# Kernel optimization log

Hardware: AMD Instinct MI355X
Metric: run time of the kernel (lower is better)

The kernel has to match this reference:

```python
import jax, jax.numpy as jnp
import numpy as np

B, L = 2, 8192
HID, HEADS, STATE, K = 1024, 16, 16, 3
HD = HID // HEADS  # head dim = 64


def setup_inputs() -> dict:
    key = jax.random.key(0)
    ks = jax.random.split(key, 4)
    u = jax.random.normal(ks[0], (B, L, 3 * HID), dtype=jnp.float32)
    short_filter_weight = jax.random.normal(ks[1], (3 * HID, 1, K), dtype=jnp.float32)
    log_poles = -jnp.abs(jax.random.normal(ks[2], (1, STATE, 1), dtype=jnp.float32))
    residues = jax.random.normal(ks[3], (1, STATE), dtype=jnp.float32)
    D = jnp.zeros((HID,), dtype=jnp.float32)
    return {"u": u, "short_filter_weight": short_filter_weight,
            "log_poles": log_poles, "residues": residues, "D": D}


def _causal_dconv(x, w):
    # x: (B, C, L), w: (C, 1, K). Cross-correlation (matches torch conv1d)
    # with left pad K-1 == torch padding=K-1 then truncating [..., :L].
    return jax.lax.conv_general_dilated(
        x, w, window_strides=(1,), padding=[(K - 1, 0)],
        dimension_numbers=("NCH", "OIH", "NCH"),
        feature_group_count=x.shape[1])


def _bidir_dconv(x, w):
    # bidirectional FIR: causal conv + anti-causal conv (same filter on the
    # time-reversed signal, reversed back), summed
    fwd = _causal_dconv(x, w)
    rev = _causal_dconv(x[..., ::-1], w)[..., ::-1]
    return fwd + rev


def _fftconv(x, H, fft_size):
    # causal long conv via 2L-point FFT (zero-padded -> linear convolution)
    X = jnp.fft.rfft(x, n=fft_size)
    return jnp.fft.irfft(X * H, n=fft_size)[..., : x.shape[-1]]


def reference(u, short_filter_weight, log_poles, residues, D):
    Bx, Lx, _ = u.shape
    u_t = jnp.transpose(u, (0, 2, 1))                 # (B, 3*HID, L)
    z_pre = _bidir_dconv(u_t, short_filter_weight)    # (B, 3*HID, L)

    # column_split: (B, HEADS, 3*HD, L) -> x2, x1, v each (B, HID, L)
    z = z_pre.reshape(Bx, HEADS, 3 * HD, Lx)
    x2 = z[:, :, :HD].reshape(Bx, HID, Lx)
    x1 = z[:, :, HD:2 * HD].reshape(Bx, HID, Lx)
    v = z[:, :, 2 * HD:].reshape(Bx, HID, Lx)
    x1v = x1 * v

    # implicit long filter from pole/residue parameterization: h (1, 1, L)
    t = jnp.arange(Lx, dtype=jnp.float32)[None, None]           # (1,1,L)
    h = (residues[..., None] * jnp.exp(log_poles * t)).sum(axis=1)[None]

    fft_size = 2 * Lx
    H = jnp.fft.rfft(h.astype(jnp.float32), n=fft_size)          # (1,1,L+1)
    # bidirectional long conv: causal + anti-causal branches
    y = (_fftconv(x1v, H, fft_size)
         + _fftconv(x1v[..., ::-1], H, fft_size)[..., ::-1])

    # skip term and output gate
    y = (y + x1v * D[:, None]) * x2                   # (B, HID, L)
    return jnp.transpose(y, (0, 2, 1))                # (B, L, HID)
```

## Files before the change

kernel.cpp:

```cpp
#include <hip/hip_runtime.h>
#include <cstdint>
#include <cstddef>


#define Bn 2
#define Ln 8192
#define HIDn 1024
#define HEADSn 16
#define STATEn 16
#define THIDn 3072

typedef __attribute__((ext_vector_type(2))) float f32x2;

__device__ __forceinline__ float ldu(const float* __restrict__ base, int t) {
    return ((unsigned)t < (unsigned)Ln) ? base[(size_t)t * THIDn] : 0.0f;
}

template <int CH>
__global__ __launch_bounds__(64, 4) void hyena_phaseA(
    const float* __restrict__ u, const float* __restrict__ sfw,
    const float* __restrict__ lp,
    float* __restrict__ carryF, float* __restrict__ carryG) {
    const int j = threadIdx.x;
    const int chunk = blockIdx.x;
    const int h = blockIdx.y;
    const int b = blockIdx.z;
    const int c1 = h * 192 + 64 + j;
    const int cv = c1 + 64;
    const int t0 = chunk * CH;
    const int t1 = t0 + CH - 1;

    const float* u1 = u + (size_t)b * Ln * THIDn + c1;
    const float* uv = u + (size_t)b * Ln * THIDn + cv;
    const float w10 = sfw[c1 * 3 + 0], w11 = sfw[c1 * 3 + 1], w12 = 2.0f * sfw[c1 * 3 + 2];
    const float wv0 = sfw[cv * 3 + 0], wv1 = sfw[cv * 3 + 1], wv2 = 2.0f * sfw[cv * 3 + 2];

    f32x2 p2[8];
#pragma unroll
    for (int i = 0; i < 8; ++i) p2[i] = (f32x2){expf(lp[2 * i]), expf(lp[2 * i + 1])};

    const int i = h * 64 + j;
    const int gch = b * HIDn + i;
    const size_t base = ((size_t)chunk * (Bn * HIDn) + gch) * 16;

    {
        f32x2 f2[8];
#pragma unroll
        for (int s = 0; s < 8; ++s) f2[s] = (f32x2){0.0f, 0.0f};
        float a0 = ldu(u1, t0 - 2), a1 = ldu(u1, t0 - 1), a2 = ldu(u1, t0), a3 = ldu(u1, t0 + 1);
        float v0 = ldu(uv, t0 - 2), v1 = ldu(uv, t0 - 1), v2 = ldu(uv, t0), v3 = ldu(uv, t0 + 1);
#pragma unroll 8
        for (int tt = 0; tt < CH; ++tt) {
            const int t = t0 + tt;
            const float a4 = ldu(u1, t + 2);
            const float v4 = ldu(uv, t + 2);
            const float z1 = fmaf(w10, a0 + a4, fmaf(w11, a1 + a3, w12 * a2));
            const float zv = fmaf(wv0, v0 + v4, fmaf(wv1, v1 + v3, wv2 * v2));
            const float x = z1 * zv;
            const f32x2 x2 = (f32x2){x, x};
#pragma unroll
            for (int s = 0; s < 8; ++s) f2[s] = __builtin_elementwise_fma(p2[s], f2[s], x2);
            a0 = a1; a1 = a2; a2 = a3; a3 = a4;
            v0 = v1; v1 = v2; v2 = v3; v3 = v4;
        }
        f32x2* cF2 = (f32x2*)(carryF + base);
#pragma unroll
        for (int s = 0; s < 8; ++s) cF2[s] = f2[s];
    }

    {
        f32x2 g2[8];
#pragma unroll
        for (int s = 0; s < 8; ++s) g2[s] = (f32x2){0.0f, 0.0f};
        float a4 = ldu(u1, t1 + 2), a3 = ldu(u1, t1 + 1), a2 = ldu(u1, t1), a1 = ldu(u1, t1 - 1);
        float v4 = ldu(uv, t1 + 2), v3 = ldu(uv, t1 + 1), v2 = ldu(uv, t1), v1 = ldu(uv, t1 - 1);
#pragma unroll 8
        for (int tt = CH - 1; tt >= 0; --tt) {
            const int t = t0 + tt;
            const float a0 = ldu(u1, t - 2);
            const float v0 = ldu(uv, t - 2);
            const float z1 = fmaf(w10, a0 + a4, fmaf(w11, a1 + a3, w12 * a2));
            const float zv = fmaf(wv0, v0 + v4, fmaf(wv1, v1 + v3, wv2 * v2));
            const float x = z1 * zv;
            const f32x2 x2 = (f32x2){x, x};
#pragma unroll
            for (int s = 0; s < 8; ++s) g2[s] = __builtin_elementwise_fma(p2[s], g2[s], x2);
            a4 = a3; a3 = a2; a2 = a1; a1 = a0;
            v4 = v3; v3 = v2; v2 = v1; v1 = v0;
        }
        f32x2* cG2 = (f32x2*)(carryG + base);
#pragma unroll
        for (int s = 0; s < 8; ++s) cG2[s] = g2[s];
    }
}

template <int CH>
__global__ __launch_bounds__(256) void hyena_phaseB(
    const float* __restrict__ lp,
    float* __restrict__ carryF, float* __restrict__ carryG) {
    constexpr int NC = Ln / CH;
    constexpr int UB = 16;
    const int dir = blockIdx.x >> 7;
    const int ht = ((blockIdx.x & 127) << 8) + threadIdx.x;
    const int s = ht & 15;
    const int gch = ht >> 4;
    const float pCH = expf(lp[s] * (float)CH);
    float c = 0.0f;
    if (dir == 0) {
        for (int k0 = 0; k0 < NC; k0 += UB) {
            float loc[UB];
#pragma unroll
            for (int q = 0; q < UB; ++q)
                loc[q] = carryF[((size_t)(k0 + q) * (Bn * HIDn) + gch) * 16 + s];
#pragma unroll
            for (int q = 0; q < UB; ++q) {
                carryF[((size_t)(k0 + q) * (Bn * HIDn) + gch) * 16 + s] = c;
                c = fmaf(pCH, c, loc[q]);
            }
        }
    } else {
        for (int k0 = NC - UB; k0 >= 0; k0 -= UB) {
            float loc[UB];
#pragma unroll
            for (int q = UB - 1; q >= 0; --q)
                loc[q] = carryG[((size_t)(k0 + q) * (Bn * HIDn) + gch) * 16 + s];
#pragma unroll
            for (int q = UB - 1; q >= 0; --q) {
                carryG[((size_t)(k0 + q) * (Bn * HIDn) + gch) * 16 + s] = c;
                c = fmaf(pCH, c, loc[q]);
            }
        }
    }
}

template <int CH>
__global__ __launch_bounds__(64, 4) void hyena_phaseC(
    const float* __restrict__ u, const float* __restrict__ sfw,
    const float* __restrict__ lp, const float* __restrict__ res,
    const float* __restrict__ Dp,
    const float* __restrict__ carryF, const float* __restrict__ carryG,
    float* __restrict__ out) {
    const int j = threadIdx.x;
    const int chunk = blockIdx.x;
    const int h = blockIdx.y;
    const int b = blockIdx.z;
    const int c2 = h * 192 + j;
    const int c1 = c2 + 64;
    const int cv = c2 + 128;
    const int i = h * 64 + j;
    const int gch = b * HIDn + i;
    const int t0 = chunk * CH;
    const int t1 = t0 + CH - 1;

    const float* u2 = u + (size_t)b * Ln * THIDn + c2;
    const float* u1 = u + (size_t)b * Ln * THIDn + c1;
    const float* uv = u + (size_t)b * Ln * THIDn + cv;
    float* op = out + (size_t)b * Ln * HIDn + i;
    const float w20 = sfw[c2 * 3 + 0], w21 = sfw[c2 * 3 + 1], w22 = 2.0f * sfw[c2 * 3 + 2];
    const float w10 = sfw[c1 * 3 + 0], w11 = sfw[c1 * 3 + 1], w12 = 2.0f * sfw[c1 * 3 + 2];
    const float wv0 = sfw[cv * 3 + 0], wv1 = sfw[cv * 3 + 1], wv2 = 2.0f * sfw[cv * 3 + 2];

    f32x2 p2[8];
#pragma unroll
    for (int s = 0; s < 8; ++s) p2[s] = (f32x2){expf(lp[2 * s]), expf(lp[2 * s + 1])};
    float rr[STATEn];
#pragma unroll
    for (int s = 0; s < STATEn; ++s) rr[s] = res[s];

    const size_t cbase = ((size_t)chunk * (Bn * HIDn) + gch) * 16;

    {
        f32x2 f2[8];
        const f32x2* cF2 = (const f32x2*)(carryF + cbase);
#pragma unroll
        for (int s = 0; s < 8; ++s) f2[s] = cF2[s];
        float a0 = ldu(u1, t0 - 2), a1 = ldu(u1, t0 - 1), a2 = ldu(u1, t0), a3 = ldu(u1, t0 + 1);
        float v0 = ldu(uv, t0 - 2), v1 = ldu(uv, t0 - 1), v2 = ldu(uv, t0), v3 = ldu(uv, t0 + 1);
#pragma unroll 8
        for (int tt = 0; tt < CH; ++tt) {
            const int t = t0 + tt;
            const float a4 = ldu(u1, t + 2);
            const float v4 = ldu(uv, t + 2);
            const float z1 = fmaf(w10, a0 + a4, fmaf(w11, a1 + a3, w12 * a2));
            const float zv = fmaf(wv0, v0 + v4, fmaf(wv1, v1 + v3, wv2 * v2));
            const float x = z1 * zv;
            const f32x2 xb = (f32x2){x, x};
#pragma unroll
            for (int s = 0; s < 8; ++s) f2[s] = __builtin_elementwise_fma(p2[s], f2[s], xb);
            float acc0 = rr[0] * f2[0].x, acc1 = rr[1] * f2[0].y;
            float acc2 = rr[2] * f2[1].x, acc3 = rr[3] * f2[1].y;
#pragma unroll
            for (int s = 2; s < 8; s += 2) {
                acc0 = fmaf(rr[2 * s + 0], f2[s].x, acc0);
                acc1 = fmaf(rr[2 * s + 1], f2[s].y, acc1);
                acc2 = fmaf(rr[2 * s + 2], f2[s + 1].x, acc2);
                acc3 = fmaf(rr[2 * s + 3], f2[s + 1].y, acc3);
            }
            op[(size_t)t * HIDn] = (acc0 + acc1) + (acc2 + acc3);
            a0 = a1; a1 = a2; a2 = a3; a3 = a4;
            v0 = v1; v1 = v2; v2 = v3; v3 = v4;
        }
    }

    {
        f32x2 g2[8];
        const f32x2* cG2 = (const f32x2*)(carryG + cbase);
#pragma unroll
        for (int s = 0; s < 8; ++s) g2[s] = cG2[s];
        const float dI = Dp[i];
        float a4 = ldu(u1, t1 + 2), a3 = ldu(u1, t1 + 1), a2 = ldu(u1, t1), a1 = ldu(u1, t1 - 1);
        float v4 = ldu(uv, t1 + 2), v3 = ldu(uv, t1 + 1), v2 = ldu(uv, t1), v1 = ldu(uv, t1 - 1);
        float e4 = ldu(u2, t1 + 2), e3 = ldu(u2, t1 + 1), e2 = ldu(u2, t1), e1 = ldu(u2, t1 - 1);
#pragma unroll 8
        for (int tt = CH - 1; tt >= 0; --tt) {
            const int t = t0 + tt;
            const float yc = op[(size_t)t * HIDn];
            const float a0 = ldu(u1, t - 2);
            const float v0 = ldu(uv, t - 2);
            const float e0 = ldu(u2, t - 2);
            const float z1 = fmaf(w10, a0 + a4, fmaf(w11, a1 + a3, w12 * a2));
            const float zv = fmaf(wv0, v0 + v4, fmaf(wv1, v1 + v3, wv2 * v2));
            const float z2 = fmaf(w20, e0 + e4, fmaf(w21, e1 + e3, w22 * e2));
            const float x = z1 * zv;
            const f32x2 xb = (f32x2){x, x};
#pragma unroll
            for (int s = 0; s < 8; ++s) g2[s] = __builtin_elementwise_fma(p2[s], g2[s], xb);
            float acc0 = rr[0] * g2[0].x, acc1 = rr[1] * g2[0].y;
            float acc2 = rr[2] * g2[1].x, acc3 = rr[3] * g2[1].y;
#pragma unroll
            for (int s = 2; s < 8; s += 2) {
                acc0 = fmaf(rr[2 * s + 0], g2[s].x, acc0);
                acc1 = fmaf(rr[2 * s + 1], g2[s].y, acc1);
                acc2 = fmaf(rr[2 * s + 2], g2[s + 1].x, acc2);
                acc3 = fmaf(rr[2 * s + 3], g2[s + 1].y, acc3);
            }
            const float ya = (acc0 + acc1) + (acc2 + acc3);
            op[(size_t)t * HIDn] = (yc + ya + dI * x) * z2;
            a4 = a3; a3 = a2; a2 = a1; a1 = a0;
            v4 = v3; v3 = v2; v2 = v1; v1 = v0;
            e4 = e3; e3 = e2; e2 = e1; e1 = e0;
        }
    }
}

template <int CH>
static void run_all(const float* u, const float* sfw, const float* lp,
                    const float* res, const float* Dp, float* out,
                    void* ws, hipStream_t stream) {
    constexpr int NC = Ln / CH;
    float* carryF = (float*)ws;
    float* carryG = carryF + (size_t)NC * (Bn * HIDn) * 16;
    dim3 grid(NC, HEADSn, Bn);
    hipLaunchKernelGGL((hyena_phaseA<CH>), grid, dim3(64), 0, stream,
                       u, sfw, lp, carryF, carryG);
    hipLaunchKernelGGL((hyena_phaseB<CH>), dim3(256), dim3(256), 0, stream,
                       lp, carryF, carryG);
    hipLaunchKernelGGL((hyena_phaseC<CH>), grid, dim3(64), 0, stream,
                       u, sfw, lp, res, Dp, carryF, carryG, out);
}

extern "C" void kernel_launch(void* const* d_in, const int* in_sizes, int n_in,
                              void* d_out, int out_size, void* d_ws, size_t ws_size,
                              hipStream_t stream) {
    const float* u   = (const float*)d_in[0];
    const float* sfw = (const float*)d_in[1];
    const float* lp  = (const float*)d_in[2];
    const float* res = (const float*)d_in[3];
    const float* Dp  = (const float*)d_in[4];
    float* out = (float*)d_out;

    const size_t need64 = ((size_t)1 << 31) / 64;
    if (ws_size >= need64)            run_all<64>(u, sfw, lp, res, Dp, out, d_ws, stream);
    else if (ws_size >= need64 / 2)   run_all<128>(u, sfw, lp, res, Dp, out, d_ws, stream);
    else if (ws_size >= need64 / 4)   run_all<256>(u, sfw, lp, res, Dp, out, d_ws, stream);
    else                              run_all<512>(u, sfw, lp, res, Dp, out, d_ws, stream);
}
```

Before: 416.3 us.

## Pack four chunks per block, drop interior bounds checks, vectorize conv, allow smaller chunks

```diff
diff --git a/kernel.cpp b/kernel.cpp
--- a/kernel.cpp
+++ b/kernel.cpp
@@ -11,87 +11,103 @@
 #define THIDn 3072
 
 typedef __attribute__((ext_vector_type(2))) float f32x2;
-
-__device__ __forceinline__ float ldu(const float* __restrict__ base, int t) {
-    return ((unsigned)t < (unsigned)Ln) ? base[(size_t)t * THIDn] : 0.0f;
+typedef __attribute__((ext_vector_type(4))) float f32x4;
+
+template <bool G>
+__device__ __forceinline__ float ldc(const float* __restrict__ base, int t) {
+    if constexpr (G) return ((unsigned)t < (unsigned)Ln) ? base[(size_t)t * THIDn] : 0.0f;
+    else return base[(size_t)t * THIDn];
+}
+
+template <int CH, bool G>
+__device__ __forceinline__ void phaseA_body(
+    const float* __restrict__ u1, const float* __restrict__ uv,
+    const f32x2 W0, const f32x2 W1, const f32x2 W2,
+    const f32x2 (&p2)[8], int t0,
+    float* __restrict__ cF, float* __restrict__ cG) {
+    const int t1 = t0 + CH - 1;
+    {
+        f32x2 f2[8];
+#pragma unroll
+        for (int s = 0; s < 8; ++s) f2[s] = (f32x2){0.0f, 0.0f};
+        f32x2 av0 = {ldc<G>(u1, t0 - 2), ldc<G>(uv, t0 - 2)};
+        f32x2 av1 = {ldc<G>(u1, t0 - 1), ldc<G>(uv, t0 - 1)};
+        f32x2 av2 = {ldc<G>(u1, t0    ), ldc<G>(uv, t0    )};
+        f32x2 av3 = {ldc<G>(u1, t0 + 1), ldc<G>(uv, t0 + 1)};
+#pragma unroll 8
+        for (int tt = 0; tt < CH; ++tt) {
+            const int t = t0 + tt;
+            const f32x2 av4 = {ldc<G>(u1, t + 2), ldc<G>(uv, t + 2)};
+            const f32x2 z = __builtin_elementwise_fma(W0, av0 + av4,
+                              __builtin_elementwise_fma(W1, av1 + av3, W2 * av2));
+            const float x = z.x * z.y;
+            const f32x2 xb = {x, x};
+#pragma unroll
+            for (int s = 0; s < 8; ++s) f2[s] = __builtin_elementwise_fma(p2[s], f2[s], xb);
+            av0 = av1; av1 = av2; av2 = av3; av3 = av4;
+        }
+        f32x4* o = (f32x4*)cF;
+#pragma unroll
+        for (int s = 0; s < 4; ++s)
+            o[s] = (f32x4){f2[2 * s].x, f2[2 * s].y, f2[2 * s + 1].x, f2[2 * s + 1].y};
+    }
+    {
+        f32x2 g2[8];
+#pragma unroll
+        for (int s = 0; s < 8; ++s) g2[s] = (f32x2){0.0f, 0.0f};
+        f32x2 av4 = {ldc<G>(u1, t1 + 2), ldc<G>(uv, t1 + 2)};
+        f32x2 av3 = {ldc<G>(u1, t1 + 1), ldc<G>(uv, t1 + 1)};
+        f32x2 av2 = {ldc<G>(u1, t1    ), ldc<G>(uv, t1    )};
+        f32x2 av1 = {ldc<G>(u1, t1 - 1), ldc<G>(uv, t1 - 1)};
+#pragma unroll 8
+        for (int tt = CH - 1; tt >= 0; --tt) {
+            const int t = t0 + tt;
+            const f32x2 av0 = {ldc<G>(u1, t - 2), ldc<G>(uv, t - 2)};
+            const f32x2 z = __builtin_elementwise_fma(W0, av0 + av4,
+                              __builtin_elementwise_fma(W1, av1 + av3, W2 * av2));
+            const float x = z.x * z.y;
+            const f32x2 xb = {x, x};
+#pragma unroll
+            for (int s = 0; s < 8; ++s) g2[s] = __builtin_elementwise_fma(p2[s], g2[s], xb);
+            av4 = av3; av3 = av2; av2 = av1; av1 = av0;
+        }
+        f32x4* o = (f32x4*)cG;
+#pragma unroll
+        for (int s = 0; s < 4; ++s)
+            o[s] = (f32x4){g2[2 * s].x, g2[2 * s].y, g2[2 * s + 1].x, g2[2 * s + 1].y};
+    }
 }
 
 template <int CH>
-__global__ __launch_bounds__(64, 4) void hyena_phaseA(
+__global__ __launch_bounds__(256, 8) void hyena_phaseA(
     const float* __restrict__ u, const float* __restrict__ sfw,
     const float* __restrict__ lp,
     float* __restrict__ carryF, float* __restrict__ carryG) {
-    const int j = threadIdx.x;
-    const int chunk = blockIdx.x;
+    constexpr int NC = Ln / CH;
+    const int lane = threadIdx.x & 63;
+    const int chunk = (blockIdx.x << 2) + (threadIdx.x >> 6);
     const int h = blockIdx.y;
     const int b = blockIdx.z;
-    const int c1 = h * 192 + 64 + j;
+    const int c1 = h * 192 + 64 + lane;
     const int cv = c1 + 64;
     const int t0 = chunk * CH;
-    const int t1 = t0 + CH - 1;
 
     const float* u1 = u + (size_t)b * Ln * THIDn + c1;
     const float* uv = u + (size_t)b * Ln * THIDn + cv;
-    const float w10 = sfw[c1 * 3 + 0], w11 = sfw[c1 * 3 + 1], w12 = 2.0f * sfw[c1 * 3 + 2];
-    const float wv0 = sfw[cv * 3 + 0], wv1 = sfw[cv * 3 + 1], wv2 = 2.0f * sfw[cv * 3 + 2];
-
+    const f32x2 W0 = {sfw[c1 * 3 + 0], sfw[cv * 3 + 0]};
+    const f32x2 W1 = {sfw[c1 * 3 + 1], sfw[cv * 3 + 1]};
+    const f32x2 W2 = {2.0f * sfw[c1 * 3 + 2], 2.0f * sfw[cv * 3 + 2]};
     f32x2 p2[8];
 #pragma unroll
-    for (int i = 0; i < 8; ++i) p2[i] = (f32x2){expf(lp[2 * i]), expf(lp[2 * i + 1])};
-
-    const int i = h * 64 + j;
-    const int gch = b * HIDn + i;
-    const size_t base = ((size_t)chunk * (Bn * HIDn) + gch) * 16;
-
-    {
-        f32x2 f2[8];
-#pragma unroll
-        for (int s = 0; s < 8; ++s) f2[s] = (f32x2){0.0f, 0.0f};
-        float a0 = ldu(u1, t0 - 2), a1 = ldu(u1, t0 - 1), a2 = ldu(u1, t0), a3 = ldu(u1, t0 + 1);
-        float v0 = ldu(uv, t0 - 2), v1 = ldu(uv, t0 - 1), v2 = ldu(uv, t0), v3 = ldu(uv, t0 + 1);
-#pragma unroll 8
-        for (int tt = 0; tt < CH; ++tt) {
-            const int t = t0 + tt;
-            const float a4 = ldu(u1, t + 2);
-            const float v4 = ldu(uv, t + 2);
-            const float z1 = fmaf(w10, a0 + a4, fmaf(w11, a1 + a3, w12 * a2));
-            const float zv = fmaf(wv0, v0 + v4, fmaf(wv1, v1 + v3, wv2 * v2));
-            const float x = z1 * zv;
-            const f32x2 x2 = (f32x2){x, x};
-#pragma unroll
-            for (int s = 0; s < 8; ++s) f2[s] = __builtin_elementwise_fma(p2[s], f2[s], x2);
-            a0 = a1; a1 = a2; a2 = a3; a3 = a4;
-            v0 = v1; v1 = v2; v2 = v3; v3 = v4;
-        }
-        f32x2* cF2 = (f32x2*)(carryF + base);
-#pragma unroll
-        for (int s = 0; s < 8; ++s) cF2[s] = f2[s];
-    }
-
-    {
-        f32x2 g2[8];
-#pragma unroll
-        for (int s = 0; s < 8; ++s) g2[s] = (f32x2){0.0f, 0.0f};
-        float a4 = ldu(u1, t1 + 2), a3 = ldu(u1, t1 + 1), a2 = ldu(u1, t1), a1 = ldu(u1, t1 - 1);
-        float v4 = ldu(uv, t1 + 2), v3 = ldu(uv, t1 + 1), v2 = ldu(uv, t1), v1 = ldu(uv, t1 - 1);
-#pragma unroll 8
-        for (int tt = CH - 1; tt >= 0; --tt) {
-            const int t = t0 + tt;
-            const float a0 = ldu(u1, t - 2);
-            const float v0 = ldu(uv, t - 2);
-            const float z1 = fmaf(w10, a0 + a4, fmaf(w11, a1 + a3, w12 * a2));
-            const float zv = fmaf(wv0, v0 + v4, fmaf(wv1, v1 + v3, wv2 * v2));
-            const float x = z1 * zv;
-            const f32x2 x2 = (f32x2){x, x};
-#pragma unroll
-            for (int s = 0; s < 8; ++s) g2[s] = __builtin_elementwise_fma(p2[s], g2[s], x2);
-            a4 = a3; a3 = a2; a2 = a1; a1 = a0;
-            v4 = v3; v3 = v2; v2 = v1; v1 = v0;
-        }
-        f32x2* cG2 = (f32x2*)(carryG + base);
-#pragma unroll
-        for (int s = 0; s < 8; ++s) cG2[s] = g2[s];
-    }
+    for (int s = 0; s < 8; ++s) p2[s] = (f32x2){expf(lp[2 * s]), expf(lp[2 * s + 1])};
+
+    const int gch = b * HIDn + h * 64 + lane;
+    const size_t cbase = ((size_t)chunk * (Bn * HIDn) + gch) * 16;
+
+    if (chunk >= 1 && chunk <= NC - 2)
+        phaseA_body<CH, false>(u1, uv, W0, W1, W2, p2, t0, carryF + cbase, carryG + cbase);
+    else
+        phaseA_body<CH, true>(u1, uv, W0, W1, W2, p2, t0, carryF + cbase, carryG + cbase);
 }
 
 template <int CH>
@@ -99,7 +115,7 @@
     const float* __restrict__ lp,
     float* __restrict__ carryF, float* __restrict__ carryG) {
     constexpr int NC = Ln / CH;
-    constexpr int UB = 16;
+    constexpr int UB = (NC >= 32) ? 32 : 16;
     const int dir = blockIdx.x >> 7;
     const int ht = ((blockIdx.x & 127) << 8) + threadIdx.x;
     const int s = ht & 15;
@@ -133,114 +149,137 @@
     }
 }
 
+template <int CH, bool G>
+__device__ __forceinline__ void phaseC_body(
+    const float* __restrict__ u2, const float* __restrict__ u1, const float* __restrict__ uv,
+    float* __restrict__ op,
+    const f32x2 W0, const f32x2 W1, const f32x2 W2,
+    const float w20, const float w21, const float w22,
+    const f32x2 (&p2)[8], const f32x2 (&rr2)[8], const float dI,
+    const float* __restrict__ cF, const float* __restrict__ cG, int t0) {
+    const int t1 = t0 + CH - 1;
+    {
+        f32x2 f2[8];
+        const f32x4* ci = (const f32x4*)cF;
+#pragma unroll
+        for (int s = 0; s < 4; ++s) {
+            const f32x4 q = ci[s];
+            f2[2 * s]     = (f32x2){q.x, q.y};
+            f2[2 * s + 1] = (f32x2){q.z, q.w};
+        }
+        f32x2 av0 = {ldc<G>(u1, t0 - 2), ldc<G>(uv, t0 - 2)};
+        f32x2 av1 = {ldc<G>(u1, t0 - 1), ldc<G>(uv, t0 - 1)};
+        f32x2 av2 = {ldc<G>(u1, t0    ), ldc<G>(uv, t0    )};
+        f32x2 av3 = {ldc<G>(u1, t0 + 1), ldc<G>(uv, t0 + 1)};
+#pragma unroll 8
+        for (int tt = 0; tt < CH; ++tt) {
+            const int t = t0 + tt;
+            const f32x2 av4 = {ldc<G>(u1, t + 2), ldc<G>(uv, t + 2)};
+            const f32x2 z = __builtin_elementwise_fma(W0, av0 + av4,
+                              __builtin_elementwise_fma(W1, av1 + av3, W2 * av2));
+            const float x = z.x * z.y;
+            const f32x2 xb = {x, x};
+#pragma unroll
+            for (int s = 0; s < 8; ++s) f2[s] = __builtin_elementwise_fma(p2[s], f2[s], xb);
+            f32x2 accA = rr2[0] * f2[0];
+            f32x2 accB = rr2[1] * f2[1];
+#pragma unroll
+            for (int s = 2; s < 8; s += 2) {
+                accA = __builtin_elementwise_fma(rr2[s], f2[s], accA);
+                accB = __builtin_elementwise_fma(rr2[s + 1], f2[s + 1], accB);
+            }
+            const f32x2 acc = accA + accB;
+            op[(size_t)t * HIDn] = acc.x + acc.y;
+            av0 = av1; av1 = av2; av2 = av3; av3 = av4;
+        }
+    }
+    {
+        f32x2 g2[8];
+        const f32x4* ci = (const f32x4*)cG;
+#pragma unroll
+        for (int s = 0; s < 4; ++s) {
+            const f32x4 q = ci[s];
+            g2[2 * s]     = (f32x2){q.x, q.y};
+            g2[2 * s + 1] = (f32x2){q.z, q.w};
+        }
+        f32x2 av4 = {ldc<G>(u1, t1 + 2), ldc<G>(uv, t1 + 2)};
+        f32x2 av3 = {ldc<G>(u1, t1 + 1), ldc<G>(uv, t1 + 1)};
+        f32x2 av2 = {ldc<G>(u1, t1    ), ldc<G>(uv, t1    )};
+        f32x2 av1 = {ldc<G>(u1, t1 - 1), ldc<G>(uv, t1 - 1)};
+        float e4 = ldc<G>(u2, t1 + 2), e3 = ldc<G>(u2, t1 + 1);
+        float e2 = ldc<G>(u2, t1), e1 = ldc<G>(u2, t1 - 1);
+#pragma unroll 8
+        for (int tt = CH - 1; tt >= 0; --tt) {
+            const int t = t0 + tt;
+            const float yc = op[(size_t)t * HIDn];
+            const f32x2 av0 = {ldc<G>(u1, t - 2), ldc<G>(uv, t - 2)};
+            const float e0 = ldc<G>(u2, t - 2);
+            const f32x2 z = __builtin_elementwise_fma(W0, av0 + av4,
+                              __builtin_elementwise_fma(W1, av1 + av3, W2 * av2));
+            const float z2 = fmaf(w20, e0 + e4, fmaf(w21, e1 + e3, w22 * e2));
+            const float x = z.x * z.y;
+            const f32x2 xb = {x, x};
+#pragma unroll
+            for (int s = 0; s < 8; ++s) g2[s] = __builtin_elementwise_fma(p2[s], g2[s], xb);
+            f32x2 accA = rr2[0] * g2[0];
+            f32x2 accB = rr2[1] * g2[1];
+#pragma unroll
+            for (int s = 2; s < 8; s += 2) {
+                accA = __builtin_elementwise_fma(rr2[s], g2[s], accA);
+                accB = __builtin_elementwise_fma(rr2[s + 1], g2[s + 1], accB);
+            }
+            const f32x2 acc = accA + accB;
+            const float ya = acc.x + acc.y;
+            op[(size_t)t * HIDn] = (yc + ya + dI * x) * z2;
+            av4 = av3; av3 = av2; av2 = av1; av1 = av0;
+            e4 = e3; e3 = e2; e2 = e1; e1 = e0;
+        }
+    }
+}
+
 template <int CH>
-__global__ __launch_bounds__(64, 4) void hyena_phaseC(
+__global__ __launch_bounds__(256, 8) void hyena_phaseC(
     const float* __restrict__ u, const float* __restrict__ sfw,
     const float* __restrict__ lp, const float* __restrict__ res,
     const float* __restrict__ Dp,
     const float* __restrict__ carryF, const float* __restrict__ carryG,
     float* __restrict__ out) {
-    const int j = threadIdx.x;
-    const int chunk = blockIdx.x;
+    constexpr int NC = Ln / CH;
+    const int lane = threadIdx.x & 63;
+    const int chunk = (blockIdx.x << 2) + (threadIdx.x >> 6);
     const int h = blockIdx.y;
     const int b = blockIdx.z;
-    const int c2 = h * 192 + j;
+    const int c2 = h * 192 + lane;
     const int c1 = c2 + 64;
     const int cv = c2 + 128;
-    const int i = h * 64 + j;
+    const int i = h * 64 + lane;
     const int gch = b * HIDn + i;
     const int t0 = chunk * CH;
-    const int t1 = t0 + CH - 1;
 
     const float* u2 = u + (size_t)b * Ln * THIDn + c2;
     const float* u1 = u + (size_t)b * Ln * THIDn + c1;
     const float* uv = u + (size_t)b * Ln * THIDn + cv;
     float* op = out + (size_t)b * Ln * HIDn + i;
     const float w20 = sfw[c2 * 3 + 0], w21 = sfw[c2 * 3 + 1], w22 = 2.0f * sfw[c2 * 3 + 2];
-    const float w10 = sfw[c1 * 3 + 0], w11 = sfw[c1 * 3 + 1], w12 = 2.0f * sfw[c1 * 3 + 2];
-    const float wv0 = sfw[cv * 3 + 0], wv1 = sfw[cv * 3 + 1], wv2 = 2.0f * sfw[cv * 3 + 2];
-
-    f32x2 p2[8];
-#pragma unroll
-    for (int s = 0; s < 8; ++s) p2[s] = (f32x2){expf(lp[2 * s]), expf(lp[2 * s + 1])};
-    float rr[STATEn];
-#pragma unroll
-    for (int s = 0; s < STATEn; ++s) rr[s] = res[s];
-
+    const f32x2 W0 = {sfw[c1 * 3 + 0], sfw[cv * 3 + 0]};
+    const f32x2 W1 = {sfw[c1 * 3 + 1], sfw[cv * 3 + 1]};
+    const f32x2 W2 = {2.0f * sfw[c1 * 3 + 2], 2.0f * sfw[cv * 3 + 2]};
+
+    f32x2 p2[8], rr2[8];
+#pragma unroll
+    for (int s = 0; s < 8; ++s) {
+        p2[s]  = (f32x2){expf(lp[2 * s]), expf(lp[2 * s + 1])};
+        rr2[s] = (f32x2){res[2 * s], res[2 * s + 1]};
+    }
+    const float dI = Dp[i];
     const size_t cbase = ((size_t)chunk * (Bn * HIDn) + gch) * 16;
 
-    {
-        f32x2 f2[8];
-        const f32x2* cF2 = (const f32x2*)(carryF + cbase);
-#pragma unroll
-        for (int s = 0; s < 8; ++s) f2[s] = cF2[s];
-        float a0 = ldu(u1, t0 - 2), a1 = ldu(u1, t0 - 1), a2 = ldu(u1, t0), a3 = ldu(u1, t0 + 1);
-        float v0 = ldu(uv, t0 - 2), v1 = ldu(uv, t0 - 1), v2 = ldu(uv, t0), v3 = ldu(uv, t0 + 1);
-#pragma unroll 8
-        for (int tt = 0; tt < CH; ++tt) {
-            const int t = t0 + tt;
-            const float a4 = ldu(u1, t + 2);
-            const float v4 = ldu(uv, t + 2);
-            const float z1 = fmaf(w10, a0 + a4, fmaf(w11, a1 + a3, w12 * a2));
-            const float zv = fmaf(wv0, v0 + v4, fmaf(wv1, v1 + v3, wv2 * v2));
-            const float x = z1 * zv;
-            const f32x2 xb = (f32x2){x, x};
-#pragma unroll
-            for (int s = 0; s < 8; ++s) f2[s] = __builtin_elementwise_fma(p2[s], f2[s], xb);
-            float acc0 = rr[0] * f2[0].x, acc1 = rr[1] * f2[0].y;
-            float acc2 = rr[2] * f2[1].x, acc3 = rr[3] * f2[1].y;
-#pragma unroll
-            for (int s = 2; s < 8; s += 2) {
-                acc0 = fmaf(rr[2 * s + 0], f2[s].x, acc0);
-                acc1 = fmaf(rr[2 * s + 1], f2[s].y, acc1);
-                acc2 = fmaf(rr[2 * s + 2], f2[s + 1].x, acc2);
-                acc3 = fmaf(rr[2 * s + 3], f2[s + 1].y, acc3);
-            }
-            op[(size_t)t * HIDn] = (acc0 + acc1) + (acc2 + acc3);
-            a0 = a1; a1 = a2; a2 = a3; a3 = a4;
-            v0 = v1; v1 = v2; v2 = v3; v3 = v4;
-        }
-    }
-
-    {
-        f32x2 g2[8];
-        const f32x2* cG2 = (const f32x2*)(carryG + cbase);
-#pragma unroll
-        for (int s = 0; s < 8; ++s) g2[s] = cG2[s];
-        const float dI = Dp[i];
-        float a4 = ldu(u1, t1 + 2), a3 = ldu(u1, t1 + 1), a2 = ldu(u1, t1), a1 = ldu(u1, t1 - 1);
-        float v4 = ldu(uv, t1 + 2), v3 = ldu(uv, t1 + 1), v2 = ldu(uv, t1), v1 = ldu(uv, t1 - 1);
-        float e4 = ldu(u2, t1 + 2), e3 = ldu(u2, t1 + 1), e2 = ldu(u2, t1), e1 = ldu(u2, t1 - 1);
-#pragma unroll 8
-        for (int tt = CH - 1; tt >= 0; --tt) {
-            const int t = t0 + tt;
-            const float yc = op[(size_t)t * HIDn];
-            const float a0 = ldu(u1, t - 2);
-            const float v0 = ldu(uv, t - 2);
-            const float e0 = ldu(u2, t - 2);
-            const float z1 = fmaf(w10, a0 + a4, fmaf(w11, a1 + a3, w12 * a2));
-            const float zv = fmaf(wv0, v0 + v4, fmaf(wv1, v1 + v3, wv2 * v2));
-            const float z2 = fmaf(w20, e0 + e4, fmaf(w21, e1 + e3, w22 * e2));
-            const float x = z1 * zv;
-            const f32x2 xb = (f32x2){x, x};
-#pragma unroll
-            for (int s = 0; s < 8; ++s) g2[s] = __builtin_elementwise_fma(p2[s], g2[s], xb);
-            float acc0 = rr[0] * g2[0].x, acc1 = rr[1] * g2[0].y;
-            float acc2 = rr[2] * g2[1].x, acc3 = rr[3] * g2[1].y;
-#pragma unroll
-            for (int s = 2; s < 8; s += 2) {
-                acc0 = fmaf(rr[2 * s + 0], g2[s].x, acc0);
-                acc1 = fmaf(rr[2 * s + 1], g2[s].y, acc1);
-                acc2 = fmaf(rr[2 * s + 2], g2[s + 1].x, acc2);
-                acc3 = fmaf(rr[2 * s + 3], g2[s + 1].y, acc3);
-            }
-            const float ya = (acc0 + acc1) + (acc2 + acc3);
-            op[(size_t)t * HIDn] = (yc + ya + dI * x) * z2;
-            a4 = a3; a3 = a2; a2 = a1; a1 = a0;
-            v4 = v3; v3 = v2; v2 = v1; v1 = v0;
-            e4 = e3; e3 = e2; e2 = e1; e1 = e0;
-        }
-    }
+    if (chunk >= 1 && chunk <= NC - 2)
+        phaseC_body<CH, false>(u2, u1, uv, op, W0, W1, W2, w20, w21, w22,
+                               p2, rr2, dI, carryF + cbase, carryG + cbase, t0);
+    else
+        phaseC_body<CH, true>(u2, u1, uv, op, W0, W1, W2, w20, w21, w22,
+                              p2, rr2, dI, carryF + cbase, carryG + cbase, t0);
 }
 
 template <int CH>
@@ -248,14 +287,15 @@
                     const float* res, const float* Dp, float* out,
                     void* ws, hipStream_t stream) {
     constexpr int NC = Ln / CH;
+    static_assert(NC % 4 == 0, "4 chunks per block");
     float* carryF = (float*)ws;
     float* carryG = carryF + (size_t)NC * (Bn * HIDn) * 16;
-    dim3 grid(NC, HEADSn, Bn);
-    hipLaunchKernelGGL((hyena_phaseA<CH>), grid, dim3(64), 0, stream,
+    dim3 grid(NC / 4, HEADSn, Bn);
+    hipLaunchKernelGGL((hyena_phaseA<CH>), grid, dim3(256), 0, stream,
                        u, sfw, lp, carryF, carryG);
     hipLaunchKernelGGL((hyena_phaseB<CH>), dim3(256), dim3(256), 0, stream,
                        lp, carryF, carryG);
-    hipLaunchKernelGGL((hyena_phaseC<CH>), grid, dim3(64), 0, stream,
+    hipLaunchKernelGGL((hyena_phaseC<CH>), grid, dim3(256), 0, stream,
                        u, sfw, lp, res, Dp, carryF, carryG, out);
 }
 
@@ -269,9 +309,10 @@
     const float* Dp  = (const float*)d_in[4];
     float* out = (float*)d_out;
 
-    const size_t need64 = ((size_t)1 << 31) / 64;
-    if (ws_size >= need64)            run_all<64>(u, sfw, lp, res, Dp, out, d_ws, stream);
-    else if (ws_size >= need64 / 2)   run_all<128>(u, sfw, lp, res, Dp, out, d_ws, stream);
-    else if (ws_size >= need64 / 4)   run_all<256>(u, sfw, lp, res, Dp, out, d_ws, stream);
+    const size_t need32 = ((size_t)1 << 31) / 32;
+    if (ws_size >= need32)            run_all<32>(u, sfw, lp, res, Dp, out, d_ws, stream);
+    else if (ws_size >= need32 / 2)   run_all<64>(u, sfw, lp, res, Dp, out, d_ws, stream);
+    else if (ws_size >= need32 / 4)   run_all<128>(u, sfw, lp, res, Dp, out, d_ws, stream);
+    else if (ws_size >= need32 / 8)   run_all<256>(u, sfw, lp, res, Dp, out, d_ws, stream);
     else                              run_all<512>(u, sfw, lp, res, Dp, out, d_ws, stream);
 }
```

New measurement: 755.1 us. 1.81x slower.
